# Optimization experiments

Hardware: AMD Instinct MI355X
Metric: run time of the kernel (lower is better)

## Reference

```python
import jax, jax.numpy as jnp
import numpy as np

NEG_SLOPE = 0.2  # PyG GATv2Conv default


def gatv2_layer(h, src, dst, Wl, bl, Wr, br, att, bias, n):
    # h: [N, din]; src/dst: [E'] (self-loops included)
    xl = h @ Wl + bl                      # [N, d] source-side transform (lin_l)
    xr = h @ Wr + br                      # [N, d] target-side transform (lin_r)
    s = xl[src] + xr[dst]                 # [E', d] per-edge gather
    e = jax.nn.leaky_relu(s, NEG_SLOPE) @ att  # [E'] GATv2 score
    # segment softmax over incoming edges of each dst node
    m = jax.ops.segment_max(e, dst, num_segments=n)
    ex = jnp.exp(e - m[dst])
    denom = jax.ops.segment_sum(ex, dst, num_segments=n)
    alpha = ex / denom[dst]               # [E']
    out = jax.ops.segment_sum(alpha[:, None] * xl[src], dst, num_segments=n)
    return out + bias                     # [N, d]


def setup_inputs() -> dict:
    key = jax.random.key(0)
    ks = jax.random.split(key, 9)
    n, e, d, L = 50000, 800000, 64, 3
    x = jax.random.normal(ks[0], (n, d), dtype=jnp.float32)
    edge_index = jax.random.randint(ks[1], (2, e), 0, n, dtype=jnp.int64)
    sc = 1.0 / np.sqrt(d)
    Wl = jax.random.normal(ks[2], (L, d, d), dtype=jnp.float32) * sc
    bl = jnp.zeros((L, d), dtype=jnp.float32)
    Wr = jax.random.normal(ks[3], (L, d, d), dtype=jnp.float32) * sc
    br = jnp.zeros((L, d), dtype=jnp.float32)
    att = jax.random.normal(ks[4], (L, d), dtype=jnp.float32) * sc
    bias = jnp.zeros((L, d), dtype=jnp.float32)
    return {"x": x, "edge_index": edge_index, "Wl": Wl, "bl": bl,
            "Wr": Wr, "br": br, "att": att, "bias": bias}


def reference(x, edge_index, Wl, bl, Wr, br, att, bias):
    n = x.shape[0]
    # PyG GATv2Conv default add_self_loops=True
    loops = jnp.arange(n, dtype=edge_index.dtype)
    src = jnp.concatenate([edge_index[0], loops])
    dst = jnp.concatenate([edge_index[1], loops])
    h = x
    num_layers = Wl.shape[0]
    for i in range(num_layers):
        h_new = jax.nn.relu(
            gatv2_layer(h, src, dst, Wl[i], bl[i], Wr[i], br[i], att[i], bias[i], n))
        # residual: applies at layer 0 too since in_dim == hidden_dim
        h = h_new + h
    return h
```

## Files before the change

kernel.cpp:

```cpp
#include <hip/hip_runtime.h>
#include <hip/hip_bf16.h>
#include <cmath>


#define D 64
#define CB 10
#define NBLK 512


__global__ __launch_bounds__(256) void hist_coarse_kernel(
    const int* __restrict__ ei, int* __restrict__ ghist, int E, int N, int NC) {
  __shared__ int h[64];
  int tid = threadIdx.x, blk = blockIdx.x;
  if (tid < 64) h[tid] = 0;
  __syncthreads();
  for (int eid = blk * 256 + tid; eid < E + N; eid += NBLK * 256) {
    int d = (eid < E) ? ei[E + eid] : (eid - E);
    atomicAdd(&h[d >> CB], 1);
  }
  __syncthreads();
  if (tid < NC) ghist[tid * NBLK + blk] = h[tid];
}

__global__ __launch_bounds__(1024) void scan_coarse_kernel(
    int* __restrict__ g, int* __restrict__ cbase, int M, int NC, int EP) {
  int tid = threadIdx.x;
  int chunk = (M + 1023) / 1024;
  int beg = tid * chunk;
  int end = min(M, beg + chunk);
  int sum = 0;
  for (int i = beg; i < end; ++i) sum += g[i];
  int lane = tid & 63, w = tid >> 6;
  int v = sum;
#pragma unroll
  for (int o = 1; o < 64; o <<= 1) {
    int t = __shfl_up(v, o, 64);
    if (lane >= o) v += t;
  }
  __shared__ int wsum[16], woff[16];
  if (lane == 63) wsum[w] = v;
  __syncthreads();
  if (tid == 0) { int r = 0; for (int i = 0; i < 16; ++i) { woff[i] = r; r += wsum[i]; } }
  __syncthreads();
  int run = woff[w] + (v - sum);
  for (int i = beg; i < end; ++i) {
    int old = g[i];
    g[i] = run;
    if ((i & (NBLK - 1)) == 0) cbase[i / NBLK] = run;
    run += old;
  }
  if (tid == 0) cbase[NC] = EP;
}

__global__ __launch_bounds__(256) void scatter_coarse_kernel(
    const int* __restrict__ ei, const int* __restrict__ g,
    unsigned* __restrict__ rec, int E, int N, int NC) {
  __shared__ int cur[64];
  int tid = threadIdx.x, blk = blockIdx.x;
  if (tid < NC) cur[tid] = g[tid * NBLK + blk];
  __syncthreads();
  for (int eid = blk * 256 + tid; eid < E + N; eid += NBLK * 256) {
    int s, d;
    if (eid < E) { s = ei[eid]; d = ei[E + eid]; }
    else         { s = d = eid - E; }
    int pos = atomicAdd(&cur[d >> CB], 1);
    rec[pos] = ((unsigned)(d & ((1 << CB) - 1)) << 16) | (unsigned)s;
  }
}

__global__ __launch_bounds__(1024) void buildcsr2_kernel(
    const unsigned* __restrict__ rec, const int* __restrict__ cbase,
    int* __restrict__ rowptr, int* __restrict__ csr_src, int N, int EP) {
  int c = blockIdx.x, tid = threadIdx.x;
  int bb = cbase[c], be = cbase[c + 1];
  __shared__ int hist[1024], cur[1024];
  hist[tid] = 0;
  __syncthreads();
  for (int p = bb + tid; p < be; p += 1024)
    atomicAdd(&hist[rec[p] >> 16], 1);
  __syncthreads();
  int dv = hist[tid];
  int lane = tid & 63, w = tid >> 6;
  int inc = dv;
#pragma unroll
  for (int o = 1; o < 64; o <<= 1) {
    int t = __shfl_up(inc, o, 64);
    if (lane >= o) inc += t;
  }
  __shared__ int wsum[16], woff[16];
  if (lane == 63) wsum[w] = inc;
  __syncthreads();
  if (tid == 0) { int r = 0; for (int i = 0; i < 16; ++i) { woff[i] = r; r += wsum[i]; } }
  __syncthreads();
  int excl = woff[w] + inc - dv;
  cur[tid] = excl;
  int node = (c << CB) + tid;
  if (node < N) rowptr[node] = bb + excl;
  if (c == 0 && tid == 0) rowptr[N] = EP;
  __syncthreads();
  for (int p = bb + tid; p < be; p += 1024) {
    unsigned r = rec[p];
    int pos = bb + atomicAdd(&cur[r >> 16], 1);
    csr_src[pos] = (int)(r & 0xFFFFu);
  }
}


__device__ __forceinline__ unsigned short f2bf(float f) {
  unsigned u = __float_as_uint(f);
  return (unsigned short)((u + 0x7FFFu + ((u >> 16) & 1u)) >> 16);
}

__global__ __launch_bounds__(256) void transform_kernel(
    const float* __restrict__ h,
    const float* __restrict__ Wl, const float* __restrict__ bl,
    const float* __restrict__ Wr, const float* __restrict__ br,
    unsigned short* __restrict__ xlh, float* __restrict__ xr, int N) {
  __shared__ float hs[16][D];
  int tid = threadIdx.x;
  int j = tid & 63;
  float wl[D], wr[D];
#pragma unroll
  for (int k = 0; k < D; ++k) {
    wl[k] = Wl[k * D + j];
    wr[k] = Wr[k * D + j];
  }
  int node0 = blockIdx.x * 16;
  for (int i = tid; i < 16 * D; i += 256) {
    int n = node0 + (i >> 6);
    hs[i >> 6][i & 63] = (n < N) ? h[(size_t)n * D + (i & 63)] : 0.f;
  }
  __syncthreads();
  float blj = bl[j], brj = br[j];
  int nl = tid >> 6;
  for (int g = 0; g < 4; ++g) {
    int local = nl * 4 + g;
    int n = node0 + local;
    float al = blj, ar = brj;
#pragma unroll
    for (int k4 = 0; k4 < D / 4; ++k4) {
      float4 hv = *reinterpret_cast<const float4*>(&hs[local][k4 * 4]);
      al = fmaf(hv.x, wl[k4 * 4 + 0], al);
      ar = fmaf(hv.x, wr[k4 * 4 + 0], ar);
      al = fmaf(hv.y, wl[k4 * 4 + 1], al);
      ar = fmaf(hv.y, wr[k4 * 4 + 1], ar);
      al = fmaf(hv.z, wl[k4 * 4 + 2], al);
      ar = fmaf(hv.z, wr[k4 * 4 + 2], ar);
      al = fmaf(hv.w, wl[k4 * 4 + 3], al);
      ar = fmaf(hv.w, wr[k4 * 4 + 3], ar);
    }
    if (n < N) {
      xlh[(size_t)n * D + j] = f2bf(al);
      xr[(size_t)n * D + j] = ar;
    }
  }
}


__global__ __launch_bounds__(256) void edge_kernel(
    const unsigned short* __restrict__ xlh, const float* __restrict__ xr,
    const float* __restrict__ h_in, const int* __restrict__ rowptr,
    const int* __restrict__ csr_src, const float* __restrict__ att,
    const float* __restrict__ bias, float* __restrict__ h_out, int N) {
  int wv = (blockIdx.x * blockDim.x + threadIdx.x) >> 6;
  int lane = threadIdx.x & 63;
  int g = lane >> 4, l16 = lane & 15;
  int v = wv * 4 + g;
  if (v >= N) return;
  float4 xr4 = *reinterpret_cast<const float4*>(&xr[(size_t)v * D + l16 * 4]);
  float4 at4 = *reinterpret_cast<const float4*>(&att[l16 * 4]);
  int beg = rowptr[v], end = rowptr[v + 1];
  int deg = end - beg;
  int glane0 = g << 4;
  float m = -INFINITY, s = 0.f;
  float ax = 0.f, ay = 0.f, az = 0.f, aw = 0.f;
  for (int sc = 0; sc < deg; sc += 16) {
    int us = csr_src[min(beg + sc + l16, end - 1)];
    int nt = min(16, deg - sc);
    for (int cc = 0; cc < nt; cc += 4) {
      float4 xu[4];
      float p[4];
#pragma unroll
      for (int k = 0; k < 4; ++k) {
        int u = __shfl(us, glane0 + cc + k, 64);
        uint2 q = *reinterpret_cast<const uint2*>(&xlh[(size_t)u * D + l16 * 4]);
        xu[k].x = __uint_as_float(q.x << 16);
        xu[k].y = __uint_as_float(q.x & 0xFFFF0000u);
        xu[k].z = __uint_as_float(q.y << 16);
        xu[k].w = __uint_as_float(q.y & 0xFFFF0000u);
        float tx = xu[k].x + xr4.x, ty = xu[k].y + xr4.y;
        float tz = xu[k].z + xr4.z, tw = xu[k].w + xr4.w;
        tx = fmaxf(tx, 0.2f * tx);
        ty = fmaxf(ty, 0.2f * ty);
        tz = fmaxf(tz, 0.2f * tz);
        tw = fmaxf(tw, 0.2f * tw);
        float pp = tx * at4.x + ty * at4.y + tz * at4.z + tw * at4.w;
        pp += __shfl_xor(pp, 1, 64);
        pp += __shfl_xor(pp, 2, 64);
        pp += __shfl_xor(pp, 4, 64);
        pp += __shfl_xor(pp, 8, 64);
        p[k] = (cc + k < nt) ? pp : -INFINITY;
      }
      float pm = fmaxf(fmaxf(p[0], p[1]), fmaxf(p[2], p[3]));
      float mn = fmaxf(m, pm);
      float a  = __expf(m - mn);
      float w0 = __expf(p[0] - mn);
      float w1 = __expf(p[1] - mn);
      float w2 = __expf(p[2] - mn);
      float w3 = __expf(p[3] - mn);
      s = s * a + (w0 + w1) + (w2 + w3);
      ax = fmaf(w0, xu[0].x, fmaf(w1, xu[1].x, fmaf(w2, xu[2].x, fmaf(w3, xu[3].x, ax * a))));
      ay = fmaf(w0, xu[0].y, fmaf(w1, xu[1].y, fmaf(w2, xu[2].y, fmaf(w3, xu[3].y, ay * a))));
      az = fmaf(w0, xu[0].z, fmaf(w1, xu[1].z, fmaf(w2, xu[2].z, fmaf(w3, xu[3].z, az * a))));
      aw = fmaf(w0, xu[0].w, fmaf(w1, xu[1].w, fmaf(w2, xu[2].w, fmaf(w3, xu[3].w, aw * a))));
      m = mn;
    }
  }
  float inv = 1.f / s;
  float4 b4v = *reinterpret_cast<const float4*>(&bias[l16 * 4]);
  float4 hv  = *reinterpret_cast<const float4*>(&h_in[(size_t)v * D + l16 * 4]);
  float4 o;
  o.x = fmaxf(ax * inv + b4v.x, 0.f) + hv.x;
  o.y = fmaxf(ay * inv + b4v.y, 0.f) + hv.y;
  o.z = fmaxf(az * inv + b4v.z, 0.f) + hv.z;
  o.w = fmaxf(aw * inv + b4v.w, 0.f) + hv.w;
  *reinterpret_cast<float4*>(&h_out[(size_t)v * D + l16 * 4]) = o;
}


extern "C" void kernel_launch(void* const* d_in, const int* in_sizes, int n_in,
                              void* d_out, int out_size, void* d_ws, size_t ws_size,
                              hipStream_t stream) {
  const float* x    = (const float*)d_in[0];
  const int*   ei   = (const int*)d_in[1];
  const float* Wl   = (const float*)d_in[2];
  const float* bl   = (const float*)d_in[3];
  const float* Wr   = (const float*)d_in[4];
  const float* br   = (const float*)d_in[5];
  const float* att  = (const float*)d_in[6];
  const float* bias = (const float*)d_in[7];

  int N = in_sizes[0] / D;
  int E = in_sizes[1] / 2;
  int L = in_sizes[2] / (D * D);
  int EP = E + N;
  int NC = (N + (1 << CB) - 1) >> CB;
  int M = NC * NBLK;

  float* xr = (float*)d_ws;
  float* hA = xr + (size_t)N * D;
  float* hB = hA + (size_t)N * D;
  unsigned short* xlh = (unsigned short*)(hB + (size_t)N * D);
  unsigned* rec = (unsigned*)(xlh + (size_t)N * D);
  int* csr_src  = (int*)(rec + EP);
  int* rowptr   = csr_src + EP;
  int* ghist    = rowptr + (N + 1);
  int* cbase    = ghist + M;

  hist_coarse_kernel<<<NBLK, 256, 0, stream>>>(ei, ghist, E, N, NC);
  scan_coarse_kernel<<<1, 1024, 0, stream>>>(ghist, cbase, M, NC, EP);
  scatter_coarse_kernel<<<NBLK, 256, 0, stream>>>(ei, ghist, rec, E, N, NC);
  buildcsr2_kernel<<<NC, 1024, 0, stream>>>(rec, cbase, rowptr, csr_src, N, EP);

  int nwaves = (N + 3) / 4;
  int nblocks = (nwaves * 64 + 255) / 256;
  const float* h_in = x;
  for (int l = 0; l < L; ++l) {
    float* h_out = (l == L - 1) ? (float*)d_out : ((l % 2 == 0) ? hA : hB);
    transform_kernel<<<(N + 15) / 16, 256, 0, stream>>>(
        h_in, Wl + (size_t)l * D * D, bl + (size_t)l * D,
        Wr + (size_t)l * D * D, br + (size_t)l * D, xlh, xr, N);
    edge_kernel<<<nblocks, 256, 0, stream>>>(
        xlh, xr, h_in, rowptr, csr_src, att + (size_t)l * D,
        bias + (size_t)l * D, h_out, N);
    h_in = h_out;
  }
}
```

Baseline: 223.4 us.

## Batch eight neighbor gathers, prefetch next index chunk, store CSR sources as 16-bit

The edge kernel now issues up to eight bf16 neighbor-row gathers before doing any score math, instead of four interleaved with compute, so more memory requests are in flight per wave. It also loads the next 16 source indices while the current chunk is being processed, which hides index-load latency. CSR source indices are stored as 16-bit values, halving index traffic and footprint. This relies on N fitting in 16 bits, as the packed record format already did, and the larger unroll raises register pressure.

```diff
diff --git a/kernel.cpp b/kernel.cpp
--- a/kernel.cpp
+++ b/kernel.cpp
@@ -70,7 +70,8 @@
 
 __global__ __launch_bounds__(1024) void buildcsr2_kernel(
     const unsigned* __restrict__ rec, const int* __restrict__ cbase,
-    int* __restrict__ rowptr, int* __restrict__ csr_src, int N, int EP) {
+    int* __restrict__ rowptr, unsigned short* __restrict__ csr_src,
+    int N, int EP) {
   int c = blockIdx.x, tid = threadIdx.x;
   int bb = cbase[c], be = cbase[c + 1];
   __shared__ int hist[1024], cur[1024];
@@ -101,7 +102,7 @@
   for (int p = bb + tid; p < be; p += 1024) {
     unsigned r = rec[p];
     int pos = bb + atomicAdd(&cur[r >> 16], 1);
-    csr_src[pos] = (int)(r & 0xFFFFu);
+    csr_src[pos] = (unsigned short)(r & 0xFFFFu);
   }
 }
 
@@ -160,7 +161,7 @@
 __global__ __launch_bounds__(256) void edge_kernel(
     const unsigned short* __restrict__ xlh, const float* __restrict__ xr,
     const float* __restrict__ h_in, const int* __restrict__ rowptr,
-    const int* __restrict__ csr_src, const float* __restrict__ att,
+    const unsigned short* __restrict__ csr_src, const float* __restrict__ att,
     const float* __restrict__ bias, float* __restrict__ h_out, int N) {
   int wv = (blockIdx.x * blockDim.x + threadIdx.x) >> 6;
   int lane = threadIdx.x & 63;
@@ -174,45 +175,62 @@
   int glane0 = g << 4;
   float m = -INFINITY, s = 0.f;
   float ax = 0.f, ay = 0.f, az = 0.f, aw = 0.f;
+  int us = csr_src[min(beg + l16, end - 1)];
   for (int sc = 0; sc < deg; sc += 16) {
-    int us = csr_src[min(beg + sc + l16, end - 1)];
+    int us_cur = us;
+    if (sc + 16 < deg)
+      us = csr_src[min(beg + sc + 16 + l16, end - 1)];
     int nt = min(16, deg - sc);
-    for (int cc = 0; cc < nt; cc += 4) {
-      float4 xu[4];
-      float p[4];
-#pragma unroll
-      for (int k = 0; k < 4; ++k) {
-        int u = __shfl(us, glane0 + cc + k, 64);
-        uint2 q = *reinterpret_cast<const uint2*>(&xlh[(size_t)u * D + l16 * 4]);
-        xu[k].x = __uint_as_float(q.x << 16);
-        xu[k].y = __uint_as_float(q.x & 0xFFFF0000u);
-        xu[k].z = __uint_as_float(q.y << 16);
-        xu[k].w = __uint_as_float(q.y & 0xFFFF0000u);
-        float tx = xu[k].x + xr4.x, ty = xu[k].y + xr4.y;
-        float tz = xu[k].z + xr4.z, tw = xu[k].w + xr4.w;
-        tx = fmaxf(tx, 0.2f * tx);
-        ty = fmaxf(ty, 0.2f * ty);
-        tz = fmaxf(tz, 0.2f * tz);
-        tw = fmaxf(tw, 0.2f * tw);
-        float pp = tx * at4.x + ty * at4.y + tz * at4.z + tw * at4.w;
-        pp += __shfl_xor(pp, 1, 64);
-        pp += __shfl_xor(pp, 2, 64);
-        pp += __shfl_xor(pp, 4, 64);
-        pp += __shfl_xor(pp, 8, 64);
-        p[k] = (cc + k < nt) ? pp : -INFINITY;
+    for (int cc = 0; cc < nt; cc += 8) {
+      int nn = nt - cc;
+      uint2 q[8];
+      float p[8];
+#pragma unroll
+      for (int k = 0; k < 8; ++k) {
+        if (k < nn) {
+          int u = __shfl(us_cur, glane0 + cc + k, 64);
+          q[k] = *reinterpret_cast<const uint2*>(&xlh[(size_t)u * D + l16 * 4]);
+        }
       }
-      float pm = fmaxf(fmaxf(p[0], p[1]), fmaxf(p[2], p[3]));
+#pragma unroll
+      for (int k = 0; k < 8; ++k) {
+        float pp = -INFINITY;
+        if (k < nn) {
+          float t0 = __uint_as_float(q[k].x << 16) + xr4.x;
+          float t1 = __uint_as_float(q[k].x & 0xFFFF0000u) + xr4.y;
+          float t2 = __uint_as_float(q[k].y << 16) + xr4.z;
+          float t3 = __uint_as_float(q[k].y & 0xFFFF0000u) + xr4.w;
+          t0 = fmaxf(t0, 0.2f * t0);
+          t1 = fmaxf(t1, 0.2f * t1);
+          t2 = fmaxf(t2, 0.2f * t2);
+          t3 = fmaxf(t3, 0.2f * t3);
+          pp = t0 * at4.x + t1 * at4.y + t2 * at4.z + t3 * at4.w;
+          pp += __shfl_xor(pp, 1, 64);
+          pp += __shfl_xor(pp, 2, 64);
+          pp += __shfl_xor(pp, 4, 64);
+          pp += __shfl_xor(pp, 8, 64);
+        }
+        p[k] = pp;
+      }
+      float pm = p[0];
+#pragma unroll
+      for (int k = 1; k < 8; ++k) pm = fmaxf(pm, p[k]);
       float mn = fmaxf(m, pm);
-      float a  = __expf(m - mn);
-      float w0 = __expf(p[0] - mn);
-      float w1 = __expf(p[1] - mn);
-      float w2 = __expf(p[2] - mn);
-      float w3 = __expf(p[3] - mn);
-      s = s * a + (w0 + w1) + (w2 + w3);
-      ax = fmaf(w0, xu[0].x, fmaf(w1, xu[1].x, fmaf(w2, xu[2].x, fmaf(w3, xu[3].x, ax * a))));
-      ay = fmaf(w0, xu[0].y, fmaf(w1, xu[1].y, fmaf(w2, xu[2].y, fmaf(w3, xu[3].y, ay * a))));
-      az = fmaf(w0, xu[0].z, fmaf(w1, xu[1].z, fmaf(w2, xu[2].z, fmaf(w3, xu[3].z, az * a))));
-      aw = fmaf(w0, xu[0].w, fmaf(w1, xu[1].w, fmaf(w2, xu[2].w, fmaf(w3, xu[3].w, aw * a))));
+      float a = __expf(m - mn);
+      float sw = 0.f;
+#pragma unroll
+      for (int k = 0; k < 8; ++k) { p[k] = __expf(p[k] - mn); sw += p[k]; }
+      s = s * a + sw;
+      ax *= a; ay *= a; az *= a; aw *= a;
+#pragma unroll
+      for (int k = 0; k < 8; ++k) {
+        if (k < nn) {
+          ax = fmaf(p[k], __uint_as_float(q[k].x << 16), ax);
+          ay = fmaf(p[k], __uint_as_float(q[k].x & 0xFFFF0000u), ay);
+          az = fmaf(p[k], __uint_as_float(q[k].y << 16), az);
+          aw = fmaf(p[k], __uint_as_float(q[k].y & 0xFFFF0000u), aw);
+        }
+      }
       m = mn;
     }
   }
@@ -252,8 +270,8 @@
   float* hB = hA + (size_t)N * D;
   unsigned short* xlh = (unsigned short*)(hB + (size_t)N * D);
   unsigned* rec = (unsigned*)(xlh + (size_t)N * D);
-  int* csr_src  = (int*)(rec + EP);
-  int* rowptr   = csr_src + EP;
+  unsigned short* csr_src = (unsigned short*)(rec + EP);
+  int* rowptr   = (int*)(csr_src + ((EP + 1) & ~1));
   int* ghist    = rowptr + (N + 1);
   int* cbase    = ghist + M;
 
```

Result: slower. 256.1 us (+14.6%).

## Assign one wave per node with 8-lane feature groups and 16-bit CSR indices

Applied to the files above, without the earlier changes.

The edge kernel now maps one 64-lane wave to each destination node instead of four nodes per wave. Each 8-lane group handles a different edge and loads 8 bf16 features with a 16-byte load, so each wave processes 16 edges per step and reduces across groups with shuffles at the end. The CSR source array is also narrowed to 16-bit indices to cut index traffic. The aim is more memory-level parallelism and shorter per-wave loops for low-degree nodes, at the cost of more cross-lane shuffle reductions and idle lanes when degrees are small. The 16-bit indices assume N fits in 16 bits, which holds for 50000 nodes.

```diff
diff --git a/kernel.cpp b/kernel.cpp
--- a/kernel.cpp
+++ b/kernel.cpp
@@ -70,7 +70,8 @@
 
 __global__ __launch_bounds__(1024) void buildcsr2_kernel(
     const unsigned* __restrict__ rec, const int* __restrict__ cbase,
-    int* __restrict__ rowptr, int* __restrict__ csr_src, int N, int EP) {
+    int* __restrict__ rowptr, unsigned short* __restrict__ csr_src,
+    int N, int EP) {
   int c = blockIdx.x, tid = threadIdx.x;
   int bb = cbase[c], be = cbase[c + 1];
   __shared__ int hist[1024], cur[1024];
@@ -101,7 +102,7 @@
   for (int p = bb + tid; p < be; p += 1024) {
     unsigned r = rec[p];
     int pos = bb + atomicAdd(&cur[r >> 16], 1);
-    csr_src[pos] = (int)(r & 0xFFFFu);
+    csr_src[pos] = (unsigned short)(r & 0xFFFFu);
   }
 }
 
@@ -157,74 +158,123 @@
 }
 
 
+__device__ __forceinline__ float bflo(unsigned u) { return __uint_as_float(u << 16); }
+__device__ __forceinline__ float bfhi(unsigned u) { return __uint_as_float(u & 0xFFFF0000u); }
+
 __global__ __launch_bounds__(256) void edge_kernel(
     const unsigned short* __restrict__ xlh, const float* __restrict__ xr,
     const float* __restrict__ h_in, const int* __restrict__ rowptr,
-    const int* __restrict__ csr_src, const float* __restrict__ att,
+    const unsigned short* __restrict__ csr_src, const float* __restrict__ att,
     const float* __restrict__ bias, float* __restrict__ h_out, int N) {
-  int wv = (blockIdx.x * blockDim.x + threadIdx.x) >> 6;
+  int v = (blockIdx.x * blockDim.x + threadIdx.x) >> 6;
+  if (v >= N) return;
   int lane = threadIdx.x & 63;
-  int g = lane >> 4, l16 = lane & 15;
-  int v = wv * 4 + g;
-  if (v >= N) return;
-  float4 xr4 = *reinterpret_cast<const float4*>(&xr[(size_t)v * D + l16 * 4]);
-  float4 at4 = *reinterpret_cast<const float4*>(&att[l16 * 4]);
+  int j8 = lane >> 3, f8 = lane & 7;
+  const float* xrp = &xr[(size_t)v * D + f8 * 8];
+  float4 xrA = *reinterpret_cast<const float4*>(xrp);
+  float4 xrB = *reinterpret_cast<const float4*>(xrp + 4);
+  float4 atA = *reinterpret_cast<const float4*>(&att[f8 * 8]);
+  float4 atB = *reinterpret_cast<const float4*>(&att[f8 * 8 + 4]);
   int beg = rowptr[v], end = rowptr[v + 1];
   int deg = end - beg;
-  int glane0 = g << 4;
   float m = -INFINITY, s = 0.f;
-  float ax = 0.f, ay = 0.f, az = 0.f, aw = 0.f;
-  for (int sc = 0; sc < deg; sc += 16) {
-    int us = csr_src[min(beg + sc + l16, end - 1)];
-    int nt = min(16, deg - sc);
-    for (int cc = 0; cc < nt; cc += 4) {
-      float4 xu[4];
-      float p[4];
-#pragma unroll
-      for (int k = 0; k < 4; ++k) {
-        int u = __shfl(us, glane0 + cc + k, 64);
-        uint2 q = *reinterpret_cast<const uint2*>(&xlh[(size_t)u * D + l16 * 4]);
-        xu[k].x = __uint_as_float(q.x << 16);
-        xu[k].y = __uint_as_float(q.x & 0xFFFF0000u);
-        xu[k].z = __uint_as_float(q.y << 16);
-        xu[k].w = __uint_as_float(q.y & 0xFFFF0000u);
-        float tx = xu[k].x + xr4.x, ty = xu[k].y + xr4.y;
-        float tz = xu[k].z + xr4.z, tw = xu[k].w + xr4.w;
-        tx = fmaxf(tx, 0.2f * tx);
-        ty = fmaxf(ty, 0.2f * ty);
-        tz = fmaxf(tz, 0.2f * tz);
-        tw = fmaxf(tw, 0.2f * tw);
-        float pp = tx * at4.x + ty * at4.y + tz * at4.z + tw * at4.w;
-        pp += __shfl_xor(pp, 1, 64);
-        pp += __shfl_xor(pp, 2, 64);
-        pp += __shfl_xor(pp, 4, 64);
-        pp += __shfl_xor(pp, 8, 64);
-        p[k] = (cc + k < nt) ? pp : -INFINITY;
-      }
-      float pm = fmaxf(fmaxf(p[0], p[1]), fmaxf(p[2], p[3]));
-      float mn = fmaxf(m, pm);
+  float4 acc0 = make_float4(0.f, 0.f, 0.f, 0.f);
+  float4 acc1 = make_float4(0.f, 0.f, 0.f, 0.f);
+  for (int base = 0; base < deg; base += 64) {
+    int us = csr_src[min(beg + base + lane, end - 1)];
+    int nb = min(64, deg - base);
+    for (int sc = 0; sc < nb; sc += 16) {
+      int j0 = sc + j8, j1 = sc + 8 + j8;
+      int u0 = __shfl(us, j0, 64);
+      int u1 = __shfl(us, j1, 64);
+      uint4 q0 = *reinterpret_cast<const uint4*>(&xlh[(size_t)u0 * D + f8 * 8]);
+      uint4 q1 = *reinterpret_cast<const uint4*>(&xlh[(size_t)u1 * D + f8 * 8]);
+      float t0, t1, t2, t3, t4, t5, t6, t7, p0, p1;
+      t0 = bflo(q0.x) + xrA.x; t1 = bfhi(q0.x) + xrA.y;
+      t2 = bflo(q0.y) + xrA.z; t3 = bfhi(q0.y) + xrA.w;
+      t4 = bflo(q0.z) + xrB.x; t5 = bfhi(q0.z) + xrB.y;
+      t6 = bflo(q0.w) + xrB.z; t7 = bfhi(q0.w) + xrB.w;
+      t0 = fmaxf(t0, 0.2f * t0); t1 = fmaxf(t1, 0.2f * t1);
+      t2 = fmaxf(t2, 0.2f * t2); t3 = fmaxf(t3, 0.2f * t3);
+      t4 = fmaxf(t4, 0.2f * t4); t5 = fmaxf(t5, 0.2f * t5);
+      t6 = fmaxf(t6, 0.2f * t6); t7 = fmaxf(t7, 0.2f * t7);
+      p0 = t0 * atA.x; p0 = fmaf(t1, atA.y, p0);
+      p0 = fmaf(t2, atA.z, p0); p0 = fmaf(t3, atA.w, p0);
+      p0 = fmaf(t4, atB.x, p0); p0 = fmaf(t5, atB.y, p0);
+      p0 = fmaf(t6, atB.z, p0); p0 = fmaf(t7, atB.w, p0);
+      t0 = bflo(q1.x) + xrA.x; t1 = bfhi(q1.x) + xrA.y;
+      t2 = bflo(q1.y) + xrA.z; t3 = bfhi(q1.y) + xrA.w;
+      t4 = bflo(q1.z) + xrB.x; t5 = bfhi(q1.z) + xrB.y;
+      t6 = bflo(q1.w) + xrB.z; t7 = bfhi(q1.w) + xrB.w;
+      t0 = fmaxf(t0, 0.2f * t0); t1 = fmaxf(t1, 0.2f * t1);
+      t2 = fmaxf(t2, 0.2f * t2); t3 = fmaxf(t3, 0.2f * t3);
+      t4 = fmaxf(t4, 0.2f * t4); t5 = fmaxf(t5, 0.2f * t5);
+      t6 = fmaxf(t6, 0.2f * t6); t7 = fmaxf(t7, 0.2f * t7);
+      p1 = t0 * atA.x; p1 = fmaf(t1, atA.y, p1);
+      p1 = fmaf(t2, atA.z, p1); p1 = fmaf(t3, atA.w, p1);
+      p1 = fmaf(t4, atB.x, p1); p1 = fmaf(t5, atB.y, p1);
+      p1 = fmaf(t6, atB.z, p1); p1 = fmaf(t7, atB.w, p1);
+      p0 += __shfl_xor(p0, 1, 64); p1 += __shfl_xor(p1, 1, 64);
+      p0 += __shfl_xor(p0, 2, 64); p1 += __shfl_xor(p1, 2, 64);
+      p0 += __shfl_xor(p0, 4, 64); p1 += __shfl_xor(p1, 4, 64);
+      p0 = (j0 < nb) ? p0 : -INFINITY;
+      p1 = (j1 < nb) ? p1 : -INFINITY;
+      float cm = fmaxf(p0, p1);
+      cm = fmaxf(cm, __shfl_xor(cm, 8, 64));
+      cm = fmaxf(cm, __shfl_xor(cm, 16, 64));
+      cm = fmaxf(cm, __shfl_xor(cm, 32, 64));
+      float mn = fmaxf(m, cm);
       float a  = __expf(m - mn);
-      float w0 = __expf(p[0] - mn);
-      float w1 = __expf(p[1] - mn);
-      float w2 = __expf(p[2] - mn);
-      float w3 = __expf(p[3] - mn);
-      s = s * a + (w0 + w1) + (w2 + w3);
-      ax = fmaf(w0, xu[0].x, fmaf(w1, xu[1].x, fmaf(w2, xu[2].x, fmaf(w3, xu[3].x, ax * a))));
-      ay = fmaf(w0, xu[0].y, fmaf(w1, xu[1].y, fmaf(w2, xu[2].y, fmaf(w3, xu[3].y, ay * a))));
-      az = fmaf(w0, xu[0].z, fmaf(w1, xu[1].z, fmaf(w2, xu[2].z, fmaf(w3, xu[3].z, az * a))));
-      aw = fmaf(w0, xu[0].w, fmaf(w1, xu[1].w, fmaf(w2, xu[2].w, fmaf(w3, xu[3].w, aw * a))));
+      float w0 = __expf(p0 - mn);
+      float w1 = __expf(p1 - mn);
+      float sw = w0 + w1;
+      sw += __shfl_xor(sw, 8, 64);
+      sw += __shfl_xor(sw, 16, 64);
+      sw += __shfl_xor(sw, 32, 64);
+      s = s * a + sw;
+      acc0.x = fmaf(w0, bflo(q0.x), fmaf(w1, bflo(q1.x), acc0.x * a));
+      acc0.y = fmaf(w0, bfhi(q0.x), fmaf(w1, bfhi(q1.x), acc0.y * a));
+      acc0.z = fmaf(w0, bflo(q0.y), fmaf(w1, bflo(q1.y), acc0.z * a));
+      acc0.w = fmaf(w0, bfhi(q0.y), fmaf(w1, bfhi(q1.y), acc0.w * a));
+      acc1.x = fmaf(w0, bflo(q0.z), fmaf(w1, bflo(q1.z), acc1.x * a));
+      acc1.y = fmaf(w0, bfhi(q0.z), fmaf(w1, bfhi(q1.z), acc1.y * a));
+      acc1.z = fmaf(w0, bflo(q0.w), fmaf(w1, bflo(q1.w), acc1.z * a));
+      acc1.w = fmaf(w0, bfhi(q0.w), fmaf(w1, bfhi(q1.w), acc1.w * a));
       m = mn;
     }
   }
-  float inv = 1.f / s;
-  float4 b4v = *reinterpret_cast<const float4*>(&bias[l16 * 4]);
-  float4 hv  = *reinterpret_cast<const float4*>(&h_in[(size_t)v * D + l16 * 4]);
-  float4 o;
-  o.x = fmaxf(ax * inv + b4v.x, 0.f) + hv.x;
-  o.y = fmaxf(ay * inv + b4v.y, 0.f) + hv.y;
-  o.z = fmaxf(az * inv + b4v.z, 0.f) + hv.z;
-  o.w = fmaxf(aw * inv + b4v.w, 0.f) + hv.w;
-  *reinterpret_cast<float4*>(&h_out[(size_t)v * D + l16 * 4]) = o;
+#pragma unroll
+  for (int o = 8; o < 64; o <<= 1) {
+    acc0.x += __shfl_xor(acc0.x, o, 64);
+    acc0.y += __shfl_xor(acc0.y, o, 64);
+    acc0.z += __shfl_xor(acc0.z, o, 64);
+    acc0.w += __shfl_xor(acc0.w, o, 64);
+    acc1.x += __shfl_xor(acc1.x, o, 64);
+    acc1.y += __shfl_xor(acc1.y, o, 64);
+    acc1.z += __shfl_xor(acc1.z, o, 64);
+    acc1.w += __shfl_xor(acc1.w, o, 64);
+  }
+  if (j8 == 0) {
+    float inv = 1.f / s;
+    const float* bp = &bias[lane * 8];
+    const float* hp = &h_in[(size_t)v * D + lane * 8];
+    float4 bA = *reinterpret_cast<const float4*>(bp);
+    float4 bB = *reinterpret_cast<const float4*>(bp + 4);
+    float4 hA = *reinterpret_cast<const float4*>(hp);
+    float4 hB = *reinterpret_cast<const float4*>(hp + 4);
+    float4 oA, oB;
+    oA.x = fmaxf(acc0.x * inv + bA.x, 0.f) + hA.x;
+    oA.y = fmaxf(acc0.y * inv + bA.y, 0.f) + hA.y;
+    oA.z = fmaxf(acc0.z * inv + bA.z, 0.f) + hA.z;
+    oA.w = fmaxf(acc0.w * inv + bA.w, 0.f) + hA.w;
+    oB.x = fmaxf(acc1.x * inv + bB.x, 0.f) + hB.x;
+    oB.y = fmaxf(acc1.y * inv + bB.y, 0.f) + hB.y;
+    oB.z = fmaxf(acc1.z * inv + bB.z, 0.f) + hB.z;
+    oB.w = fmaxf(acc1.w * inv + bB.w, 0.f) + hB.w;
+    float* op = &h_out[(size_t)v * D + lane * 8];
+    *reinterpret_cast<float4*>(op) = oA;
+    *reinterpret_cast<float4*>(op + 4) = oB;
+  }
 }
 
 
@@ -252,8 +302,8 @@
   float* hB = hA + (size_t)N * D;
   unsigned short* xlh = (unsigned short*)(hB + (size_t)N * D);
   unsigned* rec = (unsigned*)(xlh + (size_t)N * D);
-  int* csr_src  = (int*)(rec + EP);
-  int* rowptr   = csr_src + EP;
+  unsigned short* csr_src = (unsigned short*)(rec + EP);
+  int* rowptr   = (int*)(csr_src + ((EP + 1) & ~1));
   int* ghist    = rowptr + (N + 1);
   int* cbase    = ghist + M;
 
@@ -262,8 +312,7 @@
   scatter_coarse_kernel<<<NBLK, 256, 0, stream>>>(ei, ghist, rec, E, N, NC);
   buildcsr2_kernel<<<NC, 1024, 0, stream>>>(rec, cbase, rowptr, csr_src, N, EP);
 
-  int nwaves = (N + 3) / 4;
-  int nblocks = (nwaves * 64 + 255) / 256;
+  int nblocks = (N + 3) / 4;
   const float* h_in = x;
   for (int l = 0; l < L; ++l) {
     float* h_out = (l == L - 1) ? (float*)d_out : ((l % 2 == 0) ? hA : hB);
```

After: 285.3 us. +27.7%, slower.
